# Kernel optimization log

Measured on AMD Instinct MI355X. Metric: run time of the kernel, lower is better.

## Reference

```python
import jax, jax.numpy as jnp
import numpy as np

N, INV, M, K, H = 131072, 256, 256, 64, 512
EPS = 1e-6  # rms norm eps
LN_EPS = 1e-5  # torch LayerNorm default


def setup_inputs() -> dict:
    key = jax.random.key(0)
    ks = jax.random.split(key, 12)
    r = lambda i, shp, s=1.0: jax.random.normal(ks[i], shp, jnp.float32) * s
    return {
        "atomic_embeddings": r(0, (N, INV + 3 * M)),
        "mean_inv": r(1, (INV,)) * 0.1,
        "std_inv": jax.random.uniform(ks[2], (INV,), jnp.float32, 0.5, 1.5),
        "rms_gamma": jnp.ones((M,), jnp.float32),
        "W0": r(3, (M, K)),
        "W1": r(4, (M, K)),
        "W2": r(5, (M, K)),
        "w_cross": r(6, (K, K)),
        "w_dot": r(7, (K, K)),
        "ln_w": jnp.ones((K,), jnp.float32),
        "ln_b": jnp.zeros((K,), jnp.float32),
        "g_w1": r(8, (INV, H)) / np.sqrt(INV),
        "g_b1": jnp.zeros((H,), jnp.float32),
        "g_w2": r(9, (H, K)) / np.sqrt(H),
        "g_b2": jnp.zeros((K,), jnp.float32),
    }


def reference(atomic_embeddings, mean_inv, std_inv, rms_gamma, W0, W1, W2,
              w_cross, w_dot, ln_w, ln_b, g_w1, g_b1, g_w2, g_b2):
    # split invariants (0e scalars come first) / equivariants (1o vectors)
    inv = atomic_embeddings[:, :INV]                       # [N, INV]
    eq = atomic_embeddings[:, INV:].reshape(-1, M, 3)      # [N, M, 3] e3nn (mul, ir) layout

    # rescale invariants
    inv = (inv - mean_inv) / std_inv

    # equivariant RMS layer norm over the M irrep channels (norm-based)
    n2 = jnp.sum(eq * eq, axis=-1)                          # [N, M] squared vector norms
    rms = jnp.sqrt(jnp.mean(n2, axis=-1, keepdims=True) + EPS)  # [N, 1]
    eq = eq * (rms_gamma / rms)[..., None]                  # [N, M, 3]

    # o3.Linear Mx1o -> Kx1o (per-component GEMM, e3nn 1/sqrt(fan_in) path norm)
    s_lin = 1.0 / np.sqrt(M)
    x0 = jnp.einsum('nmi,mk->nki', eq, W0) * s_lin          # [N, K, 3]
    x1 = jnp.einsum('nmi,mk->nki', eq, W1) * s_lin
    x2 = jnp.einsum('nmi,mk->nki', eq, W2) * s_lin

    # tp_cross: Kx1o (x) Kx1o -> Kx1e, 'uvu' weighted, component norm.
    # CG(1,1->1) = eps_ijk/sqrt(6); path weight sqrt(dim(1e)/fan_in)=sqrt(3/K)
    # => overall 1/sqrt(2K). Contract weight into x1 first to stay O(N K^2).
    y1 = jnp.einsum('nvj,uv->nuj', x1, w_cross)             # [N, K, 3]
    cross = jnp.cross(x0, y1) / np.sqrt(2.0 * K)            # [N, K, 3] (1e)

    # tp_dot: Kx1e (x) Kx1o -> Kx0o, 'uvu' weighted, component norm.
    # CG(1,1->0) = delta_ij/sqrt(3); path weight sqrt(1/K) => 1/sqrt(3K).
    y2 = jnp.einsum('nvj,uv->nuj', x2, w_dot)               # [N, K, 3]
    chi = jnp.sum(cross * y2, axis=-1) / np.sqrt(3.0 * K)   # [N, K] pseudoscalars

    # LayerNorm over K
    mu = jnp.mean(chi, axis=-1, keepdims=True)
    var = jnp.mean(jnp.square(chi - mu), axis=-1, keepdims=True)
    out = (chi - mu) / jnp.sqrt(var + LN_EPS) * ln_w + ln_b

    # ChiGate: sigmoid(Linear(SiLU(Linear(inv))))
    gate = jax.nn.sigmoid(jax.nn.silu(inv @ g_w1 + g_b1) @ g_w2 + g_b2)
    return gate * out
```

## Files before the change

kernel.cpp:

```cpp
#include <hip/hip_runtime.h>
#include <math.h>

#define ROW_D 1024
#define INV_D 256

typedef short bf16x8 __attribute__((ext_vector_type(8)));
typedef float f32x4 __attribute__((ext_vector_type(4)));

#define MFMA16(a,b,c) __builtin_amdgcn_mfma_f32_16x16x32_bf16((a),(b),(c),0,0,0)

__device__ __forceinline__ unsigned short f2bf(float f) {
    union { float f; unsigned int u; } x; x.f = f;
    return (unsigned short)((x.u + 0x7FFFu + ((x.u >> 16) & 1u)) >> 16);
}
__device__ __forceinline__ float bf2f(unsigned short h) {
    union { unsigned int u; float f; } x; x.u = ((unsigned int)h) << 16;
    return x.f;
}

__global__ void prep_kernel(
    const float* __restrict__ g_w1, const float* __restrict__ mean_inv,
    const float* __restrict__ std_inv, const float* __restrict__ g_w2,
    const float* __restrict__ W0, const float* __restrict__ W1,
    const float* __restrict__ W2, const float* __restrict__ rms_gamma,
    const float* __restrict__ w_cross, const float* __restrict__ w_dot,
    const float* __restrict__ g_b1,
    unsigned short* __restrict__ W1t, unsigned short* __restrict__ W2t,
    unsigned short* __restrict__ Wcat, unsigned short* __restrict__ wcb,
    unsigned short* __restrict__ wdb, float* __restrict__ b1p)
{
    const int nth = gridDim.x * 256;
    for (int idx = blockIdx.x * 256 + threadIdx.x; idx < 221696; idx += nth) {
        if (idx < 131072) {
            int h = idx >> 8, m = idx & 255;
            W1t[idx] = f2bf(g_w1[m * 512 + h] / std_inv[m]);
        } else if (idx < 163840) {
            int t = idx - 131072; int k = t >> 9, h = t & 511;
            W2t[t] = f2bf(g_w2[h * 64 + k]);
        } else if (idx < 212992) {
            int t = idx - 163840; int r = t >> 8, m = t & 255;
            int tt = r >> 6, k = r & 63;
            const float* Wt = (tt == 0) ? W0 : ((tt == 1) ? W1 : W2);
            Wcat[t] = f2bf(Wt[m * 64 + k] * rms_gamma[m] * 0.0625f);
        } else if (idx < 217088) {
            int t = idx - 212992; wcb[t] = f2bf(w_cross[t]);
        } else if (idx < 221184) {
            int t = idx - 217088; wdb[t] = f2bf(w_dot[t]);
        } else {
            int h = idx - 221184;
            float s = 0.f;
            for (int m = 0; m < 256; ++m)
                s += mean_inv[m] / std_inv[m] * g_w1[m * 512 + h];
            b1p[h] = g_b1[h] - s;
        }
    }
}

__global__ __launch_bounds__(256, 2) void gate_kernel(
    const float* __restrict__ emb,
    const unsigned short* __restrict__ W1t,
    const unsigned short* __restrict__ W2t,
    const float* __restrict__ b1p,
    const float* __restrict__ g_b2,
    float* __restrict__ out)
{
    __shared__ __align__(16) char smem[46080];
    unsigned short* As   = (unsigned short*)smem;
    unsigned short* B1s  = (unsigned short*)(smem + 18432);
    unsigned short* B2s  = B1s;
    unsigned short* acts = (unsigned short*)(smem + 27648);

    const int tid = threadIdx.x;
    const int wv = tid >> 6, ln = tid & 63;
    const int lr = ln & 15, lq = ln >> 4;
    const long n0 = (long)blockIdx.x * 128;

    f32x4 acc2[2][4];
#pragma unroll
    for (int r = 0; r < 2; ++r)
#pragma unroll
        for (int c = 0; c < 4; ++c) acc2[r][c] = (f32x4){0.f, 0.f, 0.f, 0.f};

    for (int hc = 0; hc < 8; ++hc) {
        f32x4 acc1[2][4];
#pragma unroll
        for (int r = 0; r < 2; ++r)
#pragma unroll
            for (int c = 0; c < 4; ++c) acc1[r][c] = (f32x4){0.f, 0.f, 0.f, 0.f};

        for (int kb = 0; kb < 4; ++kb) {
            __syncthreads();
#pragma unroll
            for (int i = 0; i < 8; ++i) {
                int idx = tid + i * 256;
                int atom = idx >> 4;
                int c4 = (idx & 15) << 2;
                float4 v = *(const float4*)(emb + (n0 + atom) * ROW_D + kb * 64 + c4);
                ushort4 h;
                h.x = f2bf(v.x); h.y = f2bf(v.y); h.z = f2bf(v.z); h.w = f2bf(v.w);
                *(ushort4*)&As[atom * 72 + c4] = h;
            }
#pragma unroll
            for (int i = 0; i < 2; ++i) {
                int idx = tid + i * 256;
                int row = idx >> 3, c8 = (idx & 7) << 3;
                *(uint4*)&B1s[row * 72 + c8] =
                    *(const uint4*)(W1t + (hc * 64 + row) * 256 + kb * 64 + c8);
            }
            __syncthreads();
#pragma unroll
            for (int ks = 0; ks < 2; ++ks) {
                bf16x8 af[2];
#pragma unroll
                for (int r = 0; r < 2; ++r)
                    af[r] = *(const bf16x8*)&As[((wv * 2 + r) * 16 + lr) * 72 + ks * 32 + lq * 8];
#pragma unroll
                for (int c = 0; c < 4; ++c) {
                    bf16x8 bf = *(const bf16x8*)&B1s[(c * 16 + lr) * 72 + ks * 32 + lq * 8];
                    acc1[0][c] = MFMA16(af[0], bf, acc1[0][c]);
                    acc1[1][c] = MFMA16(af[1], bf, acc1[1][c]);
                }
            }
        }
        __syncthreads();
#pragma unroll
        for (int r = 0; r < 2; ++r)
#pragma unroll
            for (int c = 0; c < 4; ++c) {
                int hl = c * 16 + lr;
                float b = b1p[hc * 64 + hl];
#pragma unroll
                for (int g = 0; g < 4; ++g) {
                    int atom = (wv * 2 + r) * 16 + lq * 4 + g;
                    float v = acc1[r][c][g] + b;
                    acts[atom * 72 + hl] = f2bf(v / (1.f + __expf(-v)));
                }
            }
#pragma unroll
        for (int i = 0; i < 2; ++i) {
            int idx = tid + i * 256;
            int row = idx >> 3, c8 = (idx & 7) << 3;
            *(uint4*)&B2s[row * 72 + c8] =
                *(const uint4*)(W2t + row * 512 + hc * 64 + c8);
        }
        __syncthreads();
#pragma unroll
        for (int ks = 0; ks < 2; ++ks) {
            bf16x8 af[2];
#pragma unroll
            for (int r = 0; r < 2; ++r)
                af[r] = *(const bf16x8*)&acts[((wv * 2 + r) * 16 + lr) * 72 + ks * 32 + lq * 8];
#pragma unroll
            for (int c = 0; c < 4; ++c) {
                bf16x8 bf = *(const bf16x8*)&B2s[(c * 16 + lr) * 72 + ks * 32 + lq * 8];
                acc2[0][c] = MFMA16(af[0], bf, acc2[0][c]);
                acc2[1][c] = MFMA16(af[1], bf, acc2[1][c]);
            }
        }
    }
#pragma unroll
    for (int r = 0; r < 2; ++r)
#pragma unroll
        for (int c = 0; c < 4; ++c) {
            int k = c * 16 + lr;
            float b2v = g_b2[k];
#pragma unroll
            for (int g = 0; g < 4; ++g) {
                int atom = (wv * 2 + r) * 16 + lq * 4 + g;
                float v = acc2[r][c][g] + b2v;
                out[(n0 + atom) * 64 + k] = 1.f / (1.f + __expf(-v));
            }
        }
}

__global__ __launch_bounds__(256, 2) void chi_kernel(
    const float* __restrict__ emb,
    const unsigned short* __restrict__ Wcat,
    const unsigned short* __restrict__ wcb,
    const unsigned short* __restrict__ wdb,
    const float* __restrict__ ln_w,
    const float* __restrict__ ln_b,
    float* __restrict__ out)
{
    __shared__ __align__(16) char smem[62592];
    unsigned short* Aeq = (unsigned short*)smem;
    unsigned short* Bw  = (unsigned short*)(smem + 13824);
    unsigned short* Xl1 = (unsigned short*)smem;
    unsigned short* Xl2 = (unsigned short*)(smem + 13824);
    unsigned short* y1l = (unsigned short*)smem;
    unsigned short* y2l = (unsigned short*)(smem + 13824);
    unsigned short* x0l = (unsigned short*)(smem + 41472);
    float* chi_s = (float*)(smem + 54016);
    float* rms_s = (float*)(smem + 62464);

    const int tid = threadIdx.x;
    const int wv = tid >> 6, ln = tid & 63;
    const int lr = ln & 15, lq = ln >> 4;
    const int a_t = tid >> 3, st = tid & 7;
    const long n0 = (long)blockIdx.x * 32;

    f32x4 acc[6][3];
#pragma unroll
    for (int tr = 0; tr < 6; ++tr)
#pragma unroll
        for (int c = 0; c < 3; ++c) acc[tr][c] = (f32x4){0.f, 0.f, 0.f, 0.f};
    float sumsq = 0.f;

    for (int kb = 0; kb < 4; ++kb) {
        __syncthreads();
#pragma unroll
        for (int j = 0; j < 6; ++j) {
            int c = (st + 8 * j) * 4;
            float4 v = *(const float4*)(emb + (n0 + a_t) * ROW_D + INV_D + kb * 192 + c);
            sumsq += v.x * v.x + v.y * v.y + v.z * v.z + v.w * v.w;
            float vv[4] = {v.x, v.y, v.z, v.w};
#pragma unroll
            for (int e = 0; e < 4; ++e) {
                int col = c + e;
                int ml = col / 3;
                int ii = col - ml * 3;
                Aeq[(ii * 32 + a_t) * 72 + ml] = f2bf(vv[e]);
            }
        }
#pragma unroll
        for (int i = 0; i < 6; ++i) {
            int idx = tid + i * 256;
            int row = idx >> 3, c8 = (idx & 7) << 3;
            *(uint4*)&Bw[row * 72 + c8] =
                *(const uint4*)(Wcat + row * 256 + kb * 64 + c8);
        }
        __syncthreads();
#pragma unroll
        for (int ks = 0; ks < 2; ++ks) {
            bf16x8 bfr[3];
#pragma unroll
            for (int c = 0; c < 3; ++c)
                bfr[c] = *(const bf16x8*)&Bw[((wv * 3 + c) * 16 + lr) * 72 + ks * 32 + lq * 8];
#pragma unroll
            for (int tr = 0; tr < 6; ++tr) {
                bf16x8 af = *(const bf16x8*)&Aeq[(tr * 16 + lr) * 72 + ks * 32 + lq * 8];
#pragma unroll
                for (int c = 0; c < 3; ++c)
                    acc[tr][c] = MFMA16(af, bfr[c], acc[tr][c]);
            }
        }
    }
    sumsq += __shfl_xor(sumsq, 1);
    sumsq += __shfl_xor(sumsq, 2);
    sumsq += __shfl_xor(sumsq, 4);
    if (st == 0) rms_s[a_t] = rsqrtf(sumsq * (1.f / 256.f) + 1e-6f);
    __syncthreads();

#pragma unroll
    for (int tr = 0; tr < 6; ++tr)
#pragma unroll
        for (int c = 0; c < 3; ++c) {
            int colg = (wv * 3 + c) * 16 + lr;
            int t = colg >> 6, k = colg & 63;
#pragma unroll
            for (int g = 0; g < 4; ++g) {
                int rowg = tr * 16 + lq * 4 + g;
                int ii = rowg >> 5, atom = rowg & 31;
                unsigned short hb = f2bf(acc[tr][c][g] * rms_s[atom]);
                if (t == 0)      x0l[atom * 196 + k * 3 + ii] = hb;
                else if (t == 1) Xl1[(atom * 3 + ii) * 72 + k] = hb;
                else             Xl2[(atom * 3 + ii) * 72 + k] = hb;
            }
        }
    __syncthreads();

    const int ts = wv & 1, cp = wv >> 1;
    const unsigned short* Xs = ts ? Xl2 : Xl1;
    const unsigned short* Wg = ts ? wdb : wcb;
    f32x4 yacc[6][2];
#pragma unroll
    for (int tr = 0; tr < 6; ++tr)
#pragma unroll
        for (int c = 0; c < 2; ++c) yacc[tr][c] = (f32x4){0.f, 0.f, 0.f, 0.f};
#pragma unroll
    for (int ks = 0; ks < 2; ++ks) {
        bf16x8 bfr[2];
#pragma unroll
        for (int c = 0; c < 2; ++c)
            bfr[c] = *(const bf16x8*)(Wg + ((cp * 2 + c) * 16 + lr) * 64 + ks * 32 + lq * 8);
#pragma unroll
        for (int tr = 0; tr < 6; ++tr) {
            bf16x8 af = *(const bf16x8*)&Xs[(tr * 16 + lr) * 72 + ks * 32 + lq * 8];
#pragma unroll
            for (int c = 0; c < 2; ++c)
                yacc[tr][c] = MFMA16(af, bfr[c], yacc[tr][c]);
        }
    }
    __syncthreads();

    unsigned short* Yd = ts ? y2l : y1l;
#pragma unroll
    for (int tr = 0; tr < 6; ++tr)
#pragma unroll
        for (int c = 0; c < 2; ++c) {
            int u = (cp * 2 + c) * 16 + lr;
#pragma unroll
            for (int g = 0; g < 4; ++g) {
                int rowg = tr * 16 + lq * 4 + g;
                Yd[rowg * 72 + u] = f2bf(yacc[tr][c][g]);
            }
        }
    __syncthreads();

    const float CHI_SCALE = 1.0f / sqrtf(24576.0f);
#pragma unroll
    for (int q = 0; q < 8; ++q) {
        int u = st + 8 * q;
        float x0a = bf2f(x0l[a_t * 196 + u * 3 + 0]);
        float x0b = bf2f(x0l[a_t * 196 + u * 3 + 1]);
        float x0c = bf2f(x0l[a_t * 196 + u * 3 + 2]);
        float y1a = bf2f(y1l[(a_t * 3 + 0) * 72 + u]);
        float y1b = bf2f(y1l[(a_t * 3 + 1) * 72 + u]);
        float y1c = bf2f(y1l[(a_t * 3 + 2) * 72 + u]);
        float y2a = bf2f(y2l[(a_t * 3 + 0) * 72 + u]);
        float y2b = bf2f(y2l[(a_t * 3 + 1) * 72 + u]);
        float y2c = bf2f(y2l[(a_t * 3 + 2) * 72 + u]);
        float c0 = x0b * y1c - x0c * y1b;
        float c1 = x0c * y1a - x0a * y1c;
        float c2 = x0a * y1b - x0b * y1a;
        chi_s[a_t * 66 + u] = (c0 * y2a + c1 * y2b + c2 * y2c) * CHI_SCALE;
    }
    __syncthreads();

    float s = 0.f;
#pragma unroll
    for (int q = 0; q < 8; ++q) s += chi_s[a_t * 66 + st + 8 * q];
    s += __shfl_xor(s, 1); s += __shfl_xor(s, 2); s += __shfl_xor(s, 4);
    float mu = s * (1.f / 64.f);
    float vv = 0.f;
#pragma unroll
    for (int q = 0; q < 8; ++q) {
        float d = chi_s[a_t * 66 + st + 8 * q] - mu;
        vv += d * d;
    }
    vv += __shfl_xor(vv, 1); vv += __shfl_xor(vv, 2); vv += __shfl_xor(vv, 4);
    float isd = rsqrtf(vv * (1.f / 64.f) + 1e-5f);
#pragma unroll
    for (int q = 0; q < 8; ++q) {
        int u = st + 8 * q;
        float val = (chi_s[a_t * 66 + u] - mu) * isd * ln_w[u] + ln_b[u];
        long o = (n0 + a_t) * 64 + u;
        out[o] = out[o] * val;
    }
}

extern "C" void kernel_launch(void* const* d_in, const int* in_sizes, int n_in,
                              void* d_out, int out_size, void* d_ws, size_t ws_size,
                              hipStream_t stream)
{
    const float* emb       = (const float*)d_in[0];
    const float* mean_inv  = (const float*)d_in[1];
    const float* std_inv   = (const float*)d_in[2];
    const float* rms_gamma = (const float*)d_in[3];
    const float* W0        = (const float*)d_in[4];
    const float* W1        = (const float*)d_in[5];
    const float* W2        = (const float*)d_in[6];
    const float* w_cross   = (const float*)d_in[7];
    const float* w_dot     = (const float*)d_in[8];
    const float* ln_w      = (const float*)d_in[9];
    const float* ln_b      = (const float*)d_in[10];
    const float* g_w1      = (const float*)d_in[11];
    const float* g_b1      = (const float*)d_in[12];
    const float* g_w2      = (const float*)d_in[13];
    const float* g_b2      = (const float*)d_in[14];
    float* out = (float*)d_out;

    char* ws = (char*)d_ws;
    unsigned short* W1t  = (unsigned short*)(ws);
    unsigned short* W2t  = (unsigned short*)(ws + 262144);
    unsigned short* Wcat = (unsigned short*)(ws + 327680);
    unsigned short* wcb  = (unsigned short*)(ws + 425984);
    unsigned short* wdb  = (unsigned short*)(ws + 434176);
    float*          b1p  = (float*)(ws + 442368);

    const int N = in_sizes[0] / ROW_D;

    prep_kernel<<<128, 256, 0, stream>>>(g_w1, mean_inv, std_inv, g_w2,
                                         W0, W1, W2, rms_gamma, w_cross, w_dot,
                                         g_b1, W1t, W2t, Wcat, wcb, wdb, b1p);
    gate_kernel<<<N / 128, 256, 0, stream>>>(emb, W1t, W2t, b1p, g_b2, out);
    chi_kernel<<<N / 32, 256, 0, stream>>>(emb, Wcat, wcb, wdb, ln_w, ln_b, out);
}
```

Measured before the change: 1.039 ms.

## Restructure gate kernel: 64-atom tiles, resident A tile, weights read from global

The gate MLP kernel now processes 64 atoms per block instead of 128 and loads the full 256-wide invariant row tile into shared memory once, in place of four K-chunks. The B-operand weights for both GEMMs are read directly from global memory (L2-cached) rather than staged through LDS. Waves are arranged as a 2x2 grid over rows and columns, and occupancy is raised to 3 blocks per CU. This removes most per-chunk syncs and LDS staging of weights, at the cost of repeated global/L2 weight reads per block and twice as many blocks.

```diff
diff --git a/kernel.cpp b/kernel.cpp
--- a/kernel.cpp
+++ b/kernel.cpp
@@ -56,7 +56,7 @@
     }
 }
 
-__global__ __launch_bounds__(256, 2) void gate_kernel(
+__global__ __launch_bounds__(256, 3) void gate_kernel(
     const float* __restrict__ emb,
     const unsigned short* __restrict__ W1t,
     const unsigned short* __restrict__ W2t,
@@ -64,113 +64,106 @@
     const float* __restrict__ g_b2,
     float* __restrict__ out)
 {
-    __shared__ __align__(16) char smem[46080];
+    __shared__ __align__(16) char smem[43008];
     unsigned short* As   = (unsigned short*)smem;
-    unsigned short* B1s  = (unsigned short*)(smem + 18432);
-    unsigned short* B2s  = B1s;
-    unsigned short* acts = (unsigned short*)(smem + 27648);
+    unsigned short* acts = (unsigned short*)(smem + 33792);
 
     const int tid = threadIdx.x;
     const int wv = tid >> 6, ln = tid & 63;
     const int lr = ln & 15, lq = ln >> 4;
-    const long n0 = (long)blockIdx.x * 128;
-
-    f32x4 acc2[2][4];
+    const int wr = (wv & 1) << 1;
+    const int wc = (wv >> 1) << 1;
+    const long n0 = (long)blockIdx.x * 64;
+
+#pragma unroll
+    for (int i = 0; i < 16; ++i) {
+        int idx = tid + i * 256;
+        int atom = idx >> 6;
+        int c4 = (idx & 63) << 2;
+        float4 v = *(const float4*)(emb + (n0 + atom) * ROW_D + c4);
+        ushort4 h;
+        h.x = f2bf(v.x); h.y = f2bf(v.y); h.z = f2bf(v.z); h.w = f2bf(v.w);
+        *(ushort4*)&As[atom * 264 + c4] = h;
+    }
+    __syncthreads();
+
+    f32x4 acc2[2][2];
 #pragma unroll
     for (int r = 0; r < 2; ++r)
 #pragma unroll
-        for (int c = 0; c < 4; ++c) acc2[r][c] = (f32x4){0.f, 0.f, 0.f, 0.f};
+        for (int c = 0; c < 2; ++c) acc2[r][c] = (f32x4){0.f, 0.f, 0.f, 0.f};
 
     for (int hc = 0; hc < 8; ++hc) {
-        f32x4 acc1[2][4];
+        f32x4 acc1[2][2];
 #pragma unroll
         for (int r = 0; r < 2; ++r)
 #pragma unroll
-            for (int c = 0; c < 4; ++c) acc1[r][c] = (f32x4){0.f, 0.f, 0.f, 0.f};
-
-        for (int kb = 0; kb < 4; ++kb) {
-            __syncthreads();
-#pragma unroll
-            for (int i = 0; i < 8; ++i) {
-                int idx = tid + i * 256;
-                int atom = idx >> 4;
-                int c4 = (idx & 15) << 2;
-                float4 v = *(const float4*)(emb + (n0 + atom) * ROW_D + kb * 64 + c4);
-                ushort4 h;
-                h.x = f2bf(v.x); h.y = f2bf(v.y); h.z = f2bf(v.z); h.w = f2bf(v.w);
-                *(ushort4*)&As[atom * 72 + c4] = h;
-            }
-#pragma unroll
-            for (int i = 0; i < 2; ++i) {
-                int idx = tid + i * 256;
-                int row = idx >> 3, c8 = (idx & 7) << 3;
-                *(uint4*)&B1s[row * 72 + c8] =
-                    *(const uint4*)(W1t + (hc * 64 + row) * 256 + kb * 64 + c8);
-            }
-            __syncthreads();
-#pragma unroll
-            for (int ks = 0; ks < 2; ++ks) {
-                bf16x8 af[2];
-#pragma unroll
-                for (int r = 0; r < 2; ++r)
-                    af[r] = *(const bf16x8*)&As[((wv * 2 + r) * 16 + lr) * 72 + ks * 32 + lq * 8];
-#pragma unroll
-                for (int c = 0; c < 4; ++c) {
-                    bf16x8 bf = *(const bf16x8*)&B1s[(c * 16 + lr) * 72 + ks * 32 + lq * 8];
-                    acc1[0][c] = MFMA16(af[0], bf, acc1[0][c]);
-                    acc1[1][c] = MFMA16(af[1], bf, acc1[1][c]);
-                }
-            }
-        }
-        __syncthreads();
-#pragma unroll
-        for (int r = 0; r < 2; ++r)
-#pragma unroll
-            for (int c = 0; c < 4; ++c) {
-                int hl = c * 16 + lr;
-                float b = b1p[hc * 64 + hl];
+            for (int c = 0; c < 2; ++c) acc1[r][c] = (f32x4){0.f, 0.f, 0.f, 0.f};
+
+#pragma unroll
+        for (int ks = 0; ks < 8; ++ks) {
+            bf16x8 af[2], bf[2];
+#pragma unroll
+            for (int r = 0; r < 2; ++r)
+                af[r] = *(const bf16x8*)&As[((wr + r) * 16 + lr) * 264 + ks * 32 + lq * 8];
+#pragma unroll
+            for (int c = 0; c < 2; ++c)
+                bf[c] = *(const bf16x8*)(W1t + (hc * 64 + (wc + c) * 16 + lr) * 256
+                                              + ks * 32 + lq * 8);
+#pragma unroll
+            for (int r = 0; r < 2; ++r)
+#pragma unroll
+                for (int c = 0; c < 2; ++c)
+                    acc1[r][c] = MFMA16(af[r], bf[c], acc1[r][c]);
+        }
+
+#pragma unroll
+        for (int c = 0; c < 2; ++c) {
+            int hl = (wc + c) * 16 + lr;
+            float b = b1p[hc * 64 + hl];
+#pragma unroll
+            for (int r = 0; r < 2; ++r)
 #pragma unroll
                 for (int g = 0; g < 4; ++g) {
-                    int atom = (wv * 2 + r) * 16 + lq * 4 + g;
+                    int atom = (wr + r) * 16 + lq * 4 + g;
                     float v = acc1[r][c][g] + b;
                     acts[atom * 72 + hl] = f2bf(v / (1.f + __expf(-v)));
                 }
-            }
-#pragma unroll
-        for (int i = 0; i < 2; ++i) {
-            int idx = tid + i * 256;
-            int row = idx >> 3, c8 = (idx & 7) << 3;
-            *(uint4*)&B2s[row * 72 + c8] =
-                *(const uint4*)(W2t + row * 512 + hc * 64 + c8);
         }
         __syncthreads();
+
 #pragma unroll
         for (int ks = 0; ks < 2; ++ks) {
-            bf16x8 af[2];
-#pragma unroll
-            for (int r = 0; r < 2; ++r)
-                af[r] = *(const bf16x8*)&acts[((wv * 2 + r) * 16 + lr) * 72 + ks * 32 + lq * 8];
-#pragma unroll
-            for (int c = 0; c < 4; ++c) {
-                bf16x8 bf = *(const bf16x8*)&B2s[(c * 16 + lr) * 72 + ks * 32 + lq * 8];
-                acc2[0][c] = MFMA16(af[0], bf, acc2[0][c]);
-                acc2[1][c] = MFMA16(af[1], bf, acc2[1][c]);
-            }
-        }
-    }
-#pragma unroll
-    for (int r = 0; r < 2; ++r)
-#pragma unroll
-        for (int c = 0; c < 4; ++c) {
-            int k = c * 16 + lr;
-            float b2v = g_b2[k];
+            bf16x8 af[2], bf[2];
+#pragma unroll
+            for (int r = 0; r < 2; ++r)
+                af[r] = *(const bf16x8*)&acts[((wr + r) * 16 + lr) * 72 + ks * 32 + lq * 8];
+#pragma unroll
+            for (int c = 0; c < 2; ++c)
+                bf[c] = *(const bf16x8*)(W2t + ((wc + c) * 16 + lr) * 512
+                                              + hc * 64 + ks * 32 + lq * 8);
+#pragma unroll
+            for (int r = 0; r < 2; ++r)
+#pragma unroll
+                for (int c = 0; c < 2; ++c)
+                    acc2[r][c] = MFMA16(af[r], bf[c], acc2[r][c]);
+        }
+        __syncthreads();
+    }
+
+#pragma unroll
+    for (int c = 0; c < 2; ++c) {
+        int k = (wc + c) * 16 + lr;
+        float b2v = g_b2[k];
+#pragma unroll
+        for (int r = 0; r < 2; ++r)
 #pragma unroll
             for (int g = 0; g < 4; ++g) {
-                int atom = (wv * 2 + r) * 16 + lq * 4 + g;
+                int atom = (wr + r) * 16 + lq * 4 + g;
                 float v = acc2[r][c][g] + b2v;
                 out[(n0 + atom) * 64 + k] = 1.f / (1.f + __expf(-v));
             }
-        }
+    }
 }
 
 __global__ __launch_bounds__(256, 2) void chi_kernel(
@@ -383,6 +376,6 @@
     prep_kernel<<<128, 256, 0, stream>>>(g_w1, mean_inv, std_inv, g_w2,
                                          W0, W1, W2, rms_gamma, w_cross, w_dot,
                                          g_b1, W1t, W2t, Wcat, wcb, wdb, b1p);
-    gate_kernel<<<N / 128, 256, 0, stream>>>(emb, W1t, W2t, b1p, g_b2, out);
+    gate_kernel<<<N / 64, 256, 0, stream>>>(emb, W1t, W2t, b1p, g_b2, out);
     chi_kernel<<<N / 32, 256, 0, stream>>>(emb, Wcat, wcb, wdb, ln_w, ln_b, out);
 }
```

After: 955.5 us. 1.09x faster.
